# Kernel tuning notes

Measured on AMD Instinct MI355X. Metric: run time of the kernel, lower is better.

Reference implementation:

```python
import jax, jax.numpy as jnp
import numpy as np

N = 8192      # nodes
NIN = 128     # input feature dim
NH = 128      # hidden dim
NC = 8        # communities
CS = N // NC  # community size


def setup_inputs() -> dict:
    key = jax.random.key(0)
    k = jax.random.split(key, 6)
    seq1 = jax.random.normal(k[0], (1, N, NIN), jnp.float32)
    seq2 = jax.random.normal(k[1], (1, N, NIN), jnp.float32)
    # dense row-stochastic-ish adjacency so GCN activations stay O(1)
    adj = jax.random.uniform(k[2], (1, N, N), jnp.float32) * (2.0 / N)
    cc_label = jnp.arange(N, dtype=jnp.int32).reshape(NC, CS)  # partition of nodes
    W = jax.random.normal(k[3], (NIN, NH), jnp.float32) / np.float32(np.sqrt(NIN))
    b = jnp.zeros((NH,), jnp.float32)
    Wb = jax.random.normal(k[4], (NH, NH), jnp.float32) / np.float32(np.sqrt(NH))
    bb = jnp.zeros((), jnp.float32)
    return {"seq1": seq1, "seq2": seq2, "adj": adj, "cc_label": cc_label,
            "W": W, "b": b, "Wb": Wb, "bb": bb}


def reference(seq1, seq2, adj, cc_label, W, b, Wb, bb):
    def gcn(seq):
        fts = jnp.einsum('bnd,dh->bnh', seq, W)            # linear
        agg = jnp.einsum('bnm,bmh->bnh', adj, fts) + b     # neighborhood aggregation
        return jax.nn.relu(agg)

    h1 = gcn(seq1)[0]   # [N, NH]
    h2 = gcn(seq2)[0]   # [N, NH]

    # ragged per-community gather (communities are equal-size here)
    hg1 = h1[cc_label]  # [NC, CS, NH]
    hg2 = h2[cc_label]  # [NC, CS, NH]

    # AvgReadout (msk=None) + sigmoid -> per-community summary
    c = jax.nn.sigmoid(jnp.mean(hg1, axis=1))              # [NC, NH]

    # Discriminator: bilinear f_k(h, c) = h @ Wb @ c + bb
    cw = jnp.einsum('hk,nk->nh', Wb, c)                    # [NC, NH]
    sc1 = jnp.einsum('nch,nh->nc', hg1, cw) + bb           # [NC, CS]
    sc2 = jnp.einsum('nch,nh->nc', hg2, cw) + bb           # [NC, CS]

    # scalar scatter-back (each node written exactly once)
    flat = cc_label.reshape(-1)
    ret1 = jnp.zeros((N,), h1.dtype).at[flat].set(sc1.reshape(-1))
    ret2 = jnp.zeros((N,), h2.dtype).at[flat].set(sc2.reshape(-1))
    return jnp.concatenate([ret1, ret2])[None, :]          # [1, 2N]
```

## Files before the change

kernel.cpp:

```cpp
#include <hip/hip_runtime.h>


#define NN    8192
#define NCOLS 256
#define ASCALE 4096.0f
#define AINV  (1.0f/4096.0f)

typedef _Float16 half8 __attribute__((ext_vector_type(8)));
typedef _Float16 half4v __attribute__((ext_vector_type(4)));
typedef float    f32x4 __attribute__((ext_vector_type(4)));

__device__ __forceinline__ void gload16(const void* g, void* l) {
  __builtin_amdgcn_global_load_lds(
      (const __attribute__((address_space(1))) char*)g,
      (__attribute__((address_space(3))) char*)l, 16, 0, 0);
}

__global__ void k0_init(const int* __restrict__ cc, int* __restrict__ node_comm,
                        float* __restrict__ S) {
  int i = blockIdx.x * 256 + threadIdx.x;
  if (i < 1024) S[i] = 0.0f;
  node_comm[cc[i]] = i >> 10;
}

__global__ __launch_bounds__(256) void k1_fts(const float* __restrict__ seq1,
                                              const float* __restrict__ seq2,
                                              const float* __restrict__ W,
                                              _Float16* __restrict__ F) {
  __shared__ char lds[65536];
  _Float16* Wt  = (_Float16*)lds;
  float*    sSeq = (float*)(lds + 32768);
  const int tid = threadIdx.x;
  const int lane = tid & 63;
  const int w = tid >> 6;
  const int l15 = lane & 15;
  const int g = lane >> 4;
  const int m0 = blockIdx.x * 64;

  for (int it = 0; it < 64; ++it) {
    int idx = it * 256 + tid;
    int d = idx >> 7, hc = idx & 127;
    int byte = (hc * 256 + d * 2) ^ ((hc & 7) << 4);
    *(_Float16*)(lds + byte) = (_Float16)W[idx];
  }

  const float* seqp[2] = {seq1, seq2};
  const int srow = tid >> 5;
  const int sck = tid & 31;

  for (int s = 0; s < 2; ++s) {
    __syncthreads();
    const float* sp = seqp[s];
#pragma unroll
    for (int i = 0; i < 8; ++i) {
      int row = i * 8 + srow;
      gload16(sp + (size_t)(m0 + row) * 128 + ((sck ^ (row & 7)) << 2),
              (char*)sSeq + i * 4096 + w * 1024);
    }
    asm volatile("s_waitcnt vmcnt(0)" ::: "memory");
    __syncthreads();

    f32x4 acc[4][2] = {};
    const float4* S4 = (const float4*)sSeq;
    const float4* W4 = (const float4*)Wt;
#pragma unroll
    for (int kk = 0; kk < 4; ++kk) {
      half8 bf[2];
#pragma unroll
      for (int nf = 0; nf < 2; ++nf) {
        int col = w * 32 + nf * 16 + l15;
        float4 bv = W4[(col * 16 + kk * 4 + g) ^ (col & 7)];
        bf[nf] = *(const half8*)&bv;
      }
#pragma unroll
      for (int mf = 0; mf < 4; ++mf) {
        int row = mf * 16 + l15;
        int bidx = row * 32 + kk * 8 + g * 2;
        float4 u = S4[bidx ^ (row & 7)];
        float4 v = S4[(bidx + 1) ^ (row & 7)];
        half8 af;
#pragma unroll
        for (int j = 0; j < 4; ++j) af[j] = (_Float16)(((const float*)&u)[j]);
#pragma unroll
        for (int j = 0; j < 4; ++j) af[4 + j] = (_Float16)(((const float*)&v)[j]);
#pragma unroll
        for (int nf = 0; nf < 2; ++nf)
          acc[mf][nf] = __builtin_amdgcn_mfma_f32_16x16x32_f16(af, bf[nf], acc[mf][nf], 0, 0, 0);
      }
    }
    __syncthreads();
    _Float16* img = (_Float16*)sSeq;
#pragma unroll
    for (int mf = 0; mf < 4; ++mf)
#pragma unroll
      for (int nf = 0; nf < 2; ++nf) {
        int col = w * 32 + nf * 16 + l15;
#pragma unroll
        for (int j = 0; j < 4; ++j) {
          int kl = mf * 16 + g * 4 + j;
          img[(kl >> 5) * 4096 + col * 32 + (kl & 31)] = (_Float16)acc[mf][nf][j];
        }
      }
    __syncthreads();
    const float4* src4 = (const float4*)sSeq;
#pragma unroll
    for (int i = 0; i < 4; ++i) {
      int e = i * 256 + tid;
      int kt = e >> 9, off = e & 511;
      ((float4*)(F + (size_t)(2 * blockIdx.x + kt) * 8192))[s * 512 + off] = src4[e];
    }
  }
}

__global__ __launch_bounds__(512) void k2_gemm(const float* __restrict__ adj,
                                               const _Float16* __restrict__ F,
                                               float* __restrict__ Pp) {
  __shared__ __align__(16) _Float16 sA[2][32768];
  const int tid = threadIdx.x;
  const int lane = tid & 63;
  const int w = tid >> 6;
  const int l15 = lane & 15;
  const int g = lane >> 4;
  const int row0 = blockIdx.x * 128;
  const int ks = blockIdx.y;
  const int wm = w >> 2, wn = w & 3;

  const float* abase = adj + (size_t)(row0 + w * 16) * NN + (size_t)ks * 2048 + lane * 4;
  const _Float16* fbase = F + (size_t)(ks * 64) * 8192;

  f32x4 acc[4][4] = {};

  auto cvt_store = [&](int b, int i, float4 v) {
    int row = w * 16 + i;
    char* dst = (char*)sA[b] + row * 512 + ((lane * 8) ^ ((row & 15) << 4));
    half4v h;
    h[0] = (_Float16)(v.x * ASCALE); h[1] = (_Float16)(v.y * ASCALE);
    h[2] = (_Float16)(v.z * ASCALE); h[3] = (_Float16)(v.w * ASCALE);
    *(half4v*)dst = h;
  };

  {
    float4 pv[16];
#pragma unroll
    for (int i = 0; i < 16; ++i) pv[i] = *(const float4*)(abase + (size_t)i * NN);
#pragma unroll
    for (int i = 0; i < 16; ++i) cvt_store(0, i, pv[i]);
  }
  __syncthreads();

  int colb[4], rowb[4], rsw[4];
#pragma unroll
  for (int nf = 0; nf < 4; ++nf) colb[nf] = (wn * 64 + nf * 16 + l15) * 32 + g * 8;
#pragma unroll
  for (int mf = 0; mf < 4; ++mf) {
    int row = wm * 64 + mf * 16 + l15;
    rowb[mf] = row * 512; rsw[mf] = (row & 15) << 4;
  }

  half8 bfc[4], bfn[4];
#pragma unroll
  for (int nf = 0; nf < 4; ++nf) {
    float4 t = *(const float4*)(fbase + colb[nf]);
    bfc[nf] = *(const half8*)&t;
  }

  for (int m = 0; m < 8; ++m) {
    const int b = m & 1;
    const bool lastm = (m == 7);
    const char* ab = (const char*)sA[b];
    const float* anext = abase + (m + 1) * 256;
    float4 ba[8][2];
#pragma unroll
    for (int s = 0; s < 8; ++s) {
      if (!(lastm && s == 7)) {
        const _Float16* fb = fbase + (size_t)(m * 8 + s + 1) * 8192;
#pragma unroll
        for (int nf = 0; nf < 4; ++nf) {
          float4 t = *(const float4*)(fb + colb[nf]);
          bfn[nf] = *(const half8*)&t;
        }
      }
      if (!lastm) {
        ba[s][0] = *(const float4*)(anext + (size_t)(2 * s) * NN);
        ba[s][1] = *(const float4*)(anext + (size_t)(2 * s + 1) * NN);
      }
#pragma unroll
      for (int mf = 0; mf < 4; ++mf) {
        half8 af = *(const half8*)(ab + rowb[mf] + ((s * 64 + g * 16) ^ rsw[mf]));
#pragma unroll
        for (int nf = 0; nf < 4; ++nf)
          acc[mf][nf] = __builtin_amdgcn_mfma_f32_16x16x32_f16(af, bfc[nf], acc[mf][nf], 0, 0, 0);
      }
      if (!lastm && s >= 2) {
        cvt_store(b ^ 1, 2 * (s - 2),     ba[s - 2][0]);
        cvt_store(b ^ 1, 2 * (s - 2) + 1, ba[s - 2][1]);
      }
#pragma unroll
      for (int nf = 0; nf < 4; ++nf) bfc[nf] = bfn[nf];
    }
    if (!lastm) {
      cvt_store(b ^ 1, 12, ba[6][0]); cvt_store(b ^ 1, 13, ba[6][1]);
      cvt_store(b ^ 1, 14, ba[7][0]); cvt_store(b ^ 1, 15, ba[7][1]);
    }
    __syncthreads();
  }

#pragma unroll
  for (int mf = 0; mf < 4; ++mf)
#pragma unroll
    for (int nf = 0; nf < 4; ++nf) {
      int col = wn * 64 + nf * 16 + l15;
#pragma unroll
      for (int j = 0; j < 4; ++j) {
        int row = row0 + wm * 64 + mf * 16 + g * 4 + j;
        Pp[((size_t)ks * NN + row) * NCOLS + col] = acc[mf][nf][j];
      }
    }
}

__global__ void k2r_reduce(const float* __restrict__ Pp, const float* __restrict__ b,
                           float* __restrict__ h) {
  int gid = blockIdx.x * 256 + threadIdx.x;
  size_t base = (size_t)gid * 4;
  float4 p0 = *(const float4*)(Pp + base);
  float4 p1 = *(const float4*)(Pp + base + 2097152);
  float4 p2 = *(const float4*)(Pp + base + 4194304);
  float4 p3 = *(const float4*)(Pp + base + 6291456);
  int n0 = (int)(base & 255) & 127;
  float4 r;
  r.x = fmaxf((p0.x + p1.x + p2.x + p3.x) * AINV + b[n0],     0.f);
  r.y = fmaxf((p0.y + p1.y + p2.y + p3.y) * AINV + b[n0 + 1], 0.f);
  r.z = fmaxf((p0.z + p1.z + p2.z + p3.z) * AINV + b[n0 + 2], 0.f);
  r.w = fmaxf((p0.w + p1.w + p2.w + p3.w) * AINV + b[n0 + 3], 0.f);
  *(float4*)(h + base) = r;
}

__global__ __launch_bounds__(128) void k3a_csum(const float* __restrict__ h,
                                                const int* __restrict__ node_comm,
                                                float* __restrict__ S) {
  int hh = threadIdx.x;
  int n0 = blockIdx.x * 32;
  float a0=0,a1=0,a2=0,a3=0,a4=0,a5=0,a6=0,a7=0;
  for (int i = 0; i < 32; ++i) {
    int node = n0 + i;
    int c = node_comm[node];
    float v = h[(size_t)node * 256 + hh];
    a0 += (c == 0) ? v : 0.f;  a1 += (c == 1) ? v : 0.f;
    a2 += (c == 2) ? v : 0.f;  a3 += (c == 3) ? v : 0.f;
    a4 += (c == 4) ? v : 0.f;  a5 += (c == 5) ? v : 0.f;
    a6 += (c == 6) ? v : 0.f;  a7 += (c == 7) ? v : 0.f;
  }
  if (a0 != 0.f) atomicAdd(&S[0 * 128 + hh], a0);
  if (a1 != 0.f) atomicAdd(&S[1 * 128 + hh], a1);
  if (a2 != 0.f) atomicAdd(&S[2 * 128 + hh], a2);
  if (a3 != 0.f) atomicAdd(&S[3 * 128 + hh], a3);
  if (a4 != 0.f) atomicAdd(&S[4 * 128 + hh], a4);
  if (a5 != 0.f) atomicAdd(&S[5 * 128 + hh], a5);
  if (a6 != 0.f) atomicAdd(&S[6 * 128 + hh], a6);
  if (a7 != 0.f) atomicAdd(&S[7 * 128 + hh], a7);
}

__global__ __launch_bounds__(128) void k3b_cw(const float* __restrict__ S,
                                              const float* __restrict__ Wb,
                                              float* __restrict__ cw) {
  __shared__ float sc[128];
  int ci = blockIdx.x;
  int hh = threadIdx.x;
  float m = S[ci * 128 + hh] * (1.0f / 1024.0f);
  sc[hh] = 1.0f / (1.0f + __expf(-m));
  __syncthreads();
  const float4* wr = (const float4*)(Wb + (size_t)hh * 128);
  float acc = 0.f;
#pragma unroll 8
  for (int k4 = 0; k4 < 32; ++k4) {
    float4 wv = wr[k4];
    acc += wv.x * sc[k4 * 4 + 0] + wv.y * sc[k4 * 4 + 1]
         + wv.z * sc[k4 * 4 + 2] + wv.w * sc[k4 * 4 + 3];
  }
  cw[ci * 128 + hh] = acc;
}

__global__ __launch_bounds__(256) void k5_score(const float* __restrict__ h,
                                                const int* __restrict__ node_comm,
                                                const float* __restrict__ cw,
                                                const float* __restrict__ bbp,
                                                float* __restrict__ out) {
  int tid = threadIdx.x;
  int q = tid & 15, nl = tid >> 4;
  int node = blockIdx.x * 16 + nl;
  int c = node_comm[node];
  const float* hr = h + (size_t)node * 256;
  const float* cr = cw + c * 128;
  float4 c0 = *(const float4*)(cr + q * 8);
  float4 c1 = *(const float4*)(cr + q * 8 + 4);
  float4 a0 = *(const float4*)(hr + q * 8);
  float4 a1 = *(const float4*)(hr + q * 8 + 4);
  float p1 = a0.x*c0.x + a0.y*c0.y + a0.z*c0.z + a0.w*c0.w
           + a1.x*c1.x + a1.y*c1.y + a1.z*c1.z + a1.w*c1.w;
  float4 b0 = *(const float4*)(hr + 128 + q * 8);
  float4 b1 = *(const float4*)(hr + 128 + q * 8 + 4);
  float p2 = b0.x*c0.x + b0.y*c0.y + b0.z*c0.z + b0.w*c0.w
           + b1.x*c1.x + b1.y*c1.y + b1.z*c1.z + b1.w*c1.w;
#pragma unroll
  for (int m = 8; m >= 1; m >>= 1) {
    p1 += __shfl_xor(p1, m, 64);
    p2 += __shfl_xor(p2, m, 64);
  }
  if (q == 0) {
    float bb = bbp[0];
    out[node] = p1 + bb;
    out[8192 + node] = p2 + bb;
  }
}

extern "C" void kernel_launch(void* const* d_in, const int* in_sizes, int n_in,
                              void* d_out, int out_size, void* d_ws, size_t ws_size,
                              hipStream_t stream) {
  (void)in_sizes; (void)n_in; (void)out_size; (void)ws_size;
  const float* seq1 = (const float*)d_in[0];
  const float* seq2 = (const float*)d_in[1];
  const float* adj  = (const float*)d_in[2];
  const int*   cc   = (const int*)d_in[3];
  const float* W    = (const float*)d_in[4];
  const float* b    = (const float*)d_in[5];
  const float* Wb   = (const float*)d_in[6];
  const float* bb   = (const float*)d_in[7];
  float* out = (float*)d_out;

  char* ws = (char*)d_ws;
  _Float16* F   = (_Float16*)(ws);
  float* h      = (float*)(ws + (4u << 20));
  float* Pp     = (float*)(ws + (12u << 20));
  float* S      = (float*)(ws + (44u << 20));
  float* cw     = (float*)(ws + (44u << 20) + 4096);
  int* node_comm = (int*)(ws + (44u << 20) + 8192);

  k0_init<<<dim3(32), dim3(256), 0, stream>>>(cc, node_comm, S);
  k1_fts<<<dim3(128), dim3(256), 0, stream>>>(seq1, seq2, W, F);
  k2_gemm<<<dim3(64, 4), dim3(512), 0, stream>>>(adj, F, Pp);
  k2r_reduce<<<dim3(2048), dim3(256), 0, stream>>>(Pp, b, h);
  k3a_csum<<<dim3(256), dim3(128), 0, stream>>>(h, node_comm, S);
  k3b_cw<<<dim3(8), dim3(128), 0, stream>>>(S, Wb, cw);
  k5_score<<<dim3(512), dim3(256), 0, stream>>>(h, node_comm, cw, bb, out);
}
```

Baseline: 119.9 us.

## Fold init into fts kernel, remap GEMM blocks per XCD, use nontemporal loads

Removes the separate init kernel by folding the node_comm scatter and the S zeroing into k1_fts, which saves one launch. The split-K GEMM grid becomes 1D, and block ids are remapped so each XCD handles one K-slice and a pair of row tiles, with the aim of improving L2 locality for the F operand. Adjacency streaming, the partial-sum stores and the reduce loads now use nontemporal hints so they do not pollute the cache. The XCD mapping assumes round-robin dispatch of blocks to 8 XCDs.

```diff
diff --git a/kernel.cpp b/kernel.cpp
--- a/kernel.cpp
+++ b/kernel.cpp
@@ -16,17 +16,13 @@
       (__attribute__((address_space(3))) char*)l, 16, 0, 0);
 }
 
-__global__ void k0_init(const int* __restrict__ cc, int* __restrict__ node_comm,
-                        float* __restrict__ S) {
-  int i = blockIdx.x * 256 + threadIdx.x;
-  if (i < 1024) S[i] = 0.0f;
-  node_comm[cc[i]] = i >> 10;
-}
-
 __global__ __launch_bounds__(256) void k1_fts(const float* __restrict__ seq1,
                                               const float* __restrict__ seq2,
                                               const float* __restrict__ W,
-                                              _Float16* __restrict__ F) {
+                                              _Float16* __restrict__ F,
+                                              const int* __restrict__ cc,
+                                              int* __restrict__ node_comm,
+                                              float* __restrict__ S) {
   __shared__ char lds[65536];
   _Float16* Wt  = (_Float16*)lds;
   float*    sSeq = (float*)(lds + 32768);
@@ -37,6 +33,14 @@
   const int g = lane >> 4;
   const int m0 = blockIdx.x * 64;
 
+  if (tid < 64) {
+    int i = blockIdx.x * 64 + tid;
+    node_comm[cc[i]] = i >> 10;
+  }
+  if (blockIdx.x == 0) {
+    for (int j = tid; j < 1024; j += 256) S[j] = 0.0f;
+  }
+
   for (int it = 0; it < 64; ++it) {
     int idx = it * 256 + tid;
     int d = idx >> 7, hc = idx & 127;
@@ -121,8 +125,11 @@
   const int w = tid >> 6;
   const int l15 = lane & 15;
   const int g = lane >> 4;
-  const int row0 = blockIdx.x * 128;
-  const int ks = blockIdx.y;
+  const int id = blockIdx.x;
+  const int xcd = id & 7;
+  const int ks = xcd >> 1;
+  const int mtile = (id >> 3) * 2 + (xcd & 1);
+  const int row0 = mtile * 128;
   const int wm = w >> 2, wn = w & 3;
 
   const float* abase = adj + (size_t)(row0 + w * 16) * NN + (size_t)ks * 2048 + lane * 4;
@@ -130,19 +137,20 @@
 
   f32x4 acc[4][4] = {};
 
-  auto cvt_store = [&](int b, int i, float4 v) {
+  auto cvt_store = [&](int b, int i, f32x4 v) {
     int row = w * 16 + i;
     char* dst = (char*)sA[b] + row * 512 + ((lane * 8) ^ ((row & 15) << 4));
     half4v h;
-    h[0] = (_Float16)(v.x * ASCALE); h[1] = (_Float16)(v.y * ASCALE);
-    h[2] = (_Float16)(v.z * ASCALE); h[3] = (_Float16)(v.w * ASCALE);
+    h[0] = (_Float16)(v[0] * ASCALE); h[1] = (_Float16)(v[1] * ASCALE);
+    h[2] = (_Float16)(v[2] * ASCALE); h[3] = (_Float16)(v[3] * ASCALE);
     *(half4v*)dst = h;
   };
 
   {
-    float4 pv[16];
-#pragma unroll
-    for (int i = 0; i < 16; ++i) pv[i] = *(const float4*)(abase + (size_t)i * NN);
+    f32x4 pv[16];
+#pragma unroll
+    for (int i = 0; i < 16; ++i)
+      pv[i] = __builtin_nontemporal_load((const f32x4*)(abase + (size_t)i * NN));
 #pragma unroll
     for (int i = 0; i < 16; ++i) cvt_store(0, i, pv[i]);
   }
@@ -169,7 +177,7 @@
     const bool lastm = (m == 7);
     const char* ab = (const char*)sA[b];
     const float* anext = abase + (m + 1) * 256;
-    float4 ba[8][2];
+    f32x4 ba[8][2];
 #pragma unroll
     for (int s = 0; s < 8; ++s) {
       if (!(lastm && s == 7)) {
@@ -181,8 +189,8 @@
         }
       }
       if (!lastm) {
-        ba[s][0] = *(const float4*)(anext + (size_t)(2 * s) * NN);
-        ba[s][1] = *(const float4*)(anext + (size_t)(2 * s + 1) * NN);
+        ba[s][0] = __builtin_nontemporal_load((const f32x4*)(anext + (size_t)(2 * s) * NN));
+        ba[s][1] = __builtin_nontemporal_load((const f32x4*)(anext + (size_t)(2 * s + 1) * NN));
       }
 #pragma unroll
       for (int mf = 0; mf < 4; ++mf) {
@@ -213,7 +221,8 @@
 #pragma unroll
       for (int j = 0; j < 4; ++j) {
         int row = row0 + wm * 64 + mf * 16 + g * 4 + j;
-        Pp[((size_t)ks * NN + row) * NCOLS + col] = acc[mf][nf][j];
+        __builtin_nontemporal_store(acc[mf][nf][j],
+            Pp + ((size_t)ks * NN + row) * NCOLS + col);
       }
     }
 }
@@ -222,16 +231,16 @@
                            float* __restrict__ h) {
   int gid = blockIdx.x * 256 + threadIdx.x;
   size_t base = (size_t)gid * 4;
-  float4 p0 = *(const float4*)(Pp + base);
-  float4 p1 = *(const float4*)(Pp + base + 2097152);
-  float4 p2 = *(const float4*)(Pp + base + 4194304);
-  float4 p3 = *(const float4*)(Pp + base + 6291456);
+  f32x4 p0 = __builtin_nontemporal_load((const f32x4*)(Pp + base));
+  f32x4 p1 = __builtin_nontemporal_load((const f32x4*)(Pp + base + 2097152));
+  f32x4 p2 = __builtin_nontemporal_load((const f32x4*)(Pp + base + 4194304));
+  f32x4 p3 = __builtin_nontemporal_load((const f32x4*)(Pp + base + 6291456));
   int n0 = (int)(base & 255) & 127;
   float4 r;
-  r.x = fmaxf((p0.x + p1.x + p2.x + p3.x) * AINV + b[n0],     0.f);
-  r.y = fmaxf((p0.y + p1.y + p2.y + p3.y) * AINV + b[n0 + 1], 0.f);
-  r.z = fmaxf((p0.z + p1.z + p2.z + p3.z) * AINV + b[n0 + 2], 0.f);
-  r.w = fmaxf((p0.w + p1.w + p2.w + p3.w) * AINV + b[n0 + 3], 0.f);
+  r.x = fmaxf((p0[0] + p1[0] + p2[0] + p3[0]) * AINV + b[n0],     0.f);
+  r.y = fmaxf((p0[1] + p1[1] + p2[1] + p3[1]) * AINV + b[n0 + 1], 0.f);
+  r.z = fmaxf((p0[2] + p1[2] + p2[2] + p3[2]) * AINV + b[n0 + 2], 0.f);
+  r.w = fmaxf((p0[3] + p1[3] + p2[3] + p3[3]) * AINV + b[n0 + 3], 0.f);
   *(float4*)(h + base) = r;
 }
 
@@ -335,9 +344,8 @@
   float* cw     = (float*)(ws + (44u << 20) + 4096);
   int* node_comm = (int*)(ws + (44u << 20) + 8192);
 
-  k0_init<<<dim3(32), dim3(256), 0, stream>>>(cc, node_comm, S);
-  k1_fts<<<dim3(128), dim3(256), 0, stream>>>(seq1, seq2, W, F);
-  k2_gemm<<<dim3(64, 4), dim3(512), 0, stream>>>(adj, F, Pp);
+  k1_fts<<<dim3(128), dim3(256), 0, stream>>>(seq1, seq2, W, F, cc, node_comm, S);
+  k2_gemm<<<dim3(256), dim3(512), 0, stream>>>(adj, F, Pp);
   k2r_reduce<<<dim3(2048), dim3(256), 0, stream>>>(Pp, b, h);
   k3a_csum<<<dim3(256), dim3(128), 0, stream>>>(h, node_comm, S);
   k3b_cw<<<dim3(8), dim3(128), 0, stream>>>(S, Wb, cw);
```

New measurement: 108.9 us. -9.2%, faster.
